# Optimization experiments

Hardware: AMD Instinct MI355X
Metric: run time of the kernel (lower is better)

## Reference

```python
import jax, jax.numpy as jnp
import numpy as np

N_NODES = 100000
N_EDGES = 1600000
D_IN = 13      # per-localization feature dim
D_POS = 3
HIDDEN = 64
D_OUT = 64


def setup_inputs() -> dict:
    key = jax.random.key(0)
    ks = jax.random.split(key, 6)
    x_locs = jax.random.normal(ks[0], (N_NODES, D_IN), dtype=jnp.float32)
    pos_locs = jax.random.uniform(ks[1], (N_NODES, D_POS), dtype=jnp.float32)
    edge_index = jax.random.randint(ks[2], (2, N_EDGES), 0, N_NODES, dtype=jnp.int64)
    fan1 = D_IN + D_POS
    W1 = jax.random.normal(ks[3], (fan1, HIDDEN), dtype=jnp.float32) / np.sqrt(fan1)
    b1 = jnp.zeros((HIDDEN,), dtype=jnp.float32)
    W2 = jax.random.normal(ks[4], (HIDDEN, D_OUT), dtype=jnp.float32) / np.sqrt(HIDDEN)
    b2 = jnp.zeros((D_OUT,), dtype=jnp.float32)
    return {"x_locs": x_locs, "pos_locs": pos_locs, "W1": W1, "b1": b1,
            "W2": W2, "b2": b2, "edge_index": edge_index}


def reference(x_locs, pos_locs, W1, b1, W2, b2, edge_index):
    # PointNetConv (source_to_target): j = edge_index[0] (source), i = edge_index[1] (target)
    src = edge_index[0]
    dst = edge_index[1]
    # message input: [x_j, pos_j - pos_i]  -> [E, D_IN + D_POS]
    msg_in = jnp.concatenate([x_locs[src], pos_locs[src] - pos_locs[dst]], axis=-1)
    # local_nn: Linear -> ReLU -> Linear
    h = jax.nn.relu(msg_in @ W1 + b1)            # [E, HIDDEN]
    h = h @ W2 + b2                               # [E, D_OUT]
    # max aggregation per target node; empty segments get -inf
    agg = jax.ops.segment_max(h, dst, num_segments=N_NODES)  # [N, D_OUT]
    # final .relu() in LocEncoder; also maps empty (-inf) segments to 0 (PyG convention)
    return jax.nn.relu(agg)
```

## Files before the change

### kernel.cpp

```cpp
#include <hip/hip_runtime.h>


#define N_NODES 100000
#define N_EDGES 1600000
#define NB2  1563
#define NBLK 391
#define BATCH 4096
#define SCAP2 1280

typedef _Float16 half8 __attribute__((ext_vector_type(8)));
typedef float float4v __attribute__((ext_vector_type(4)));

__device__ inline int wave_incl_scan(int v, int lane) {
#pragma unroll
    for (int d = 1; d < 64; d <<= 1) {
        const int t = __shfl_up(v, d);
        if (lane >= d) v += t;
    }
    return v;
}

__global__ __launch_bounds__(256) void precompute_kernel(
    const float* __restrict__ x, const float* __restrict__ pos,
    const float* __restrict__ W1, const float* __restrict__ b1,
    _Float16* __restrict__ u16, _Float16* __restrict__ w16)
{
    const int lane = threadIdx.x & 63;
    float w1c[16];
#pragma unroll
    for (int k = 0; k < 16; ++k) w1c[k] = W1[k * 64 + lane];
    const float b1c = b1[lane];

    const int waveId = blockIdx.x * 4 + (threadIdx.x >> 6);
    const int step   = 512 * 4 * 2;

    for (int nd = waveId * 2; nd < N_NODES; nd += step) {
        const int nA = nd, nB = nd + 1;
        float mA = 0.f, mB = 0.f;
        if (lane < 13) {
            mA = x[nA * 13 + lane];
            mB = x[nB * 13 + lane];
        } else if (lane < 16) {
            mA = pos[nA * 3 + (lane - 13)];
            mB = pos[nB * 3 + (lane - 13)];
        }

        float aA = b1c, wA = 0.f, aB = b1c, wB = 0.f;
#pragma unroll
        for (int k = 0; k < 13; ++k) {
            aA = fmaf(__shfl(mA, k), w1c[k], aA);
            aB = fmaf(__shfl(mB, k), w1c[k], aB);
        }
#pragma unroll
        for (int k = 13; k < 16; ++k) {
            const float pA = __shfl(mA, k), pB = __shfl(mB, k);
            aA = fmaf(pA, w1c[k], aA);  wA = fmaf(pA, w1c[k], wA);
            aB = fmaf(pB, w1c[k], aB);  wB = fmaf(pB, w1c[k], wB);
        }
        u16[nA * 64 + lane] = (_Float16)aA;
        w16[nA * 64 + lane] = (_Float16)wA;
        u16[nB * 64 + lane] = (_Float16)aB;
        w16[nB * 64 + lane] = (_Float16)wB;
    }
}

__global__ __launch_bounds__(256) void partition_kernel(
    const int* __restrict__ ei,
    int* __restrict__ offsT,
    int* __restrict__ blockSorted)
{
    __shared__ int hist[NB2], eoff[NB2], offc[NB2];
    __shared__ int csumP[25];

    const int tid  = threadIdx.x;
    const int lane = tid & 63;
    const int wv   = tid >> 6;
    const int blk  = blockIdx.x;
    const int e0   = blk * BATCH;
    const int nn   = (N_EDGES - e0) < BATCH ? (N_EDGES - e0) : BATCH;

    for (int i = tid; i < NB2; i += 256) hist[i] = 0;
    __syncthreads();

#pragma unroll
    for (int rep = 0; rep < 4; ++rep) {
        const int base = rep * 1024 + tid * 4;
        if (base < nn) {
            const int4 d4 = *(const int4*)(ei + N_EDGES + e0 + base);
            atomicAdd(&hist[d4.x >> 6], 1);
            atomicAdd(&hist[d4.y >> 6], 1);
            atomicAdd(&hist[d4.z >> 6], 1);
            atomicAdd(&hist[d4.w >> 6], 1);
        }
    }
    __syncthreads();

    for (int c = wv; c < 25; c += 4) {
        const int idx = c * 64 + lane;
        const int val = (idx < NB2) ? hist[idx] : 0;
        const int inc = wave_incl_scan(val, lane);
        if (idx < NB2) eoff[idx] = inc;
        if (lane == 63) csumP[c] = inc;
    }
    __syncthreads();
    if (tid == 0) {
        int a = 0;
#pragma unroll
        for (int c = 0; c < 25; ++c) { const int t = csumP[c]; csumP[c] = a; a += t; }
    }
    __syncthreads();
    for (int c = wv; c < 25; c += 4) {
        const int idx = c * 64 + lane;
        if (idx < NB2) eoff[idx] += csumP[c] - hist[idx];
    }
    __syncthreads();

    for (int b = tid; b < NB2; b += 256) {
        offsT[b * NBLK + blk] = eoff[b];
        offc[b] = eoff[b];
    }
    if (tid == 0) offsT[NB2 * NBLK + blk] = nn;
    __syncthreads();

    int* dstp = blockSorted + blk * BATCH;
#pragma unroll
    for (int rep = 0; rep < 4; ++rep) {
        const int base = rep * 1024 + tid * 4;
        if (base < nn) {
            const int4 s4 = *(const int4*)(ei + e0 + base);
            const int4 d4 = *(const int4*)(ei + N_EDGES + e0 + base);
            int p;
            p = atomicAdd(&offc[d4.x >> 6], 1); dstp[p] = (s4.x << 6) | (d4.x & 63);
            p = atomicAdd(&offc[d4.y >> 6], 1); dstp[p] = (s4.y << 6) | (d4.y & 63);
            p = atomicAdd(&offc[d4.z >> 6], 1); dstp[p] = (s4.z << 6) | (d4.z & 63);
            p = atomicAdd(&offc[d4.w >> 6], 1); dstp[p] = (s4.w << 6) | (d4.w & 63);
        }
    }
}

__global__ __launch_bounds__(256, 4) void aggregate_kernel(
    const _Float16* __restrict__ u16,
    const _Float16* __restrict__ w16,
    const float* __restrict__ W2,
    const float* __restrict__ b2,
    const int*   __restrict__ offsT,
    const int*   __restrict__ blockSorted,
    float*       __restrict__ out)
{
    __shared__ int staged[SCAP2];
    __shared__ int sortedL[SCAP2];
    __shared__ int E[NBLK], G[NBLK];
    __shared__ int hist[64], nstart[64], hoff[64];
    __shared__ int csum[8];
    __shared__ int totT;

    const int tid  = threadIdx.x;
    const int lane = tid & 63;
    const int wv   = tid >> 6;
    const int q = lane >> 4, n = lane & 15;
    const int b = blockIdx.x;
    const int node0 = b * 64;

    half8 w2f[2][4];
#pragma unroll
    for (int s = 0; s < 2; ++s)
#pragma unroll
        for (int t = 0; t < 4; ++t)
#pragma unroll
            for (int j = 0; j < 8; ++j)
                w2f[s][t][j] = (_Float16)W2[(s * 32 + q * 8 + j) * 64 + (n + 16 * t)];
    float b2c[4];
#pragma unroll
    for (int t = 0; t < 4; ++t) b2c[t] = b2[n + 16 * t];

    if (tid < 64) hist[tid] = 0;

    for (int r = tid; r < NBLK; r += 256) {
        const int lo = offsT[b * NBLK + r];
        const int hi = offsT[(b + 1) * NBLK + r];
        staged[r] = hi - lo;
        G[r] = r * BATCH + lo;
    }
    __syncthreads();
    for (int c = wv; c < 7; c += 4) {
        const int idx = c * 64 + lane;
        const int val = (idx < NBLK) ? staged[idx] : 0;
        const int inc = wave_incl_scan(val, lane);
        if (idx < NBLK) E[idx] = inc;
        if (lane == 63) csum[c] = inc;
    }
    __syncthreads();
    if (tid == 0) {
        int a = 0;
#pragma unroll
        for (int c = 0; c < 7; ++c) { const int t = csum[c]; csum[c] = a; a += t; }
        totT = a;
    }
    __syncthreads();
    for (int c = wv; c < 7; c += 4) {
        const int idx = c * 64 + lane;
        if (idx < NBLK) E[idx] += csum[c] - staged[idx];
    }
    __syncthreads();

    int T = totT; T = T < SCAP2 ? T : SCAP2;

    for (int i = tid; i < T; i += 256) {
        int lo = 0, hi = NBLK - 1;
#pragma unroll
        for (int s = 0; s < 9; ++s) {
            const int mid = (lo + hi + 1) >> 1;
            if (E[mid] <= i) lo = mid; else hi = mid - 1;
        }
        const int w = blockSorted[G[lo] + (i - E[lo])];
        staged[i] = w;
        atomicAdd(&hist[w & 63], 1);
    }
    __syncthreads();

    if (wv == 0) {
        const int v = hist[lane];
        const int inc = wave_incl_scan(v, lane);
        nstart[lane] = inc - v;
        hoff[lane]   = inc - v;
    }
    __syncthreads();
    for (int i = tid; i < T; i += 256) {
        const int w = staged[i];
        const int p = atomicAdd(&hoff[w & 63], 1);
        sortedL[p] = w >> 6;
    }
    __syncthreads();

    const half8 zero8 = {0, 0, 0, 0, 0, 0, 0, 0};

    auto compute = [&](int node, int2 sd, int src,
                       half8 ulo, half8 uhi, half8 wl, half8 wh) {
        float vmax[4] = {0.f, 0.f, 0.f, 0.f};
        int base = 0;
        while (true) {
            const int rows = (sd.y - base) < 16 ? (sd.y - base) : 16;
            if (rows > 0) {
                const half8 alo = __builtin_elementwise_max(ulo - wl, zero8);
                const half8 ahi = __builtin_elementwise_max(uhi - wh, zero8);
                float4v c2[4];
#pragma unroll
                for (int t = 0; t < 4; ++t) {
                    c2[t] = __builtin_amdgcn_mfma_f32_16x16x32_f16(
                        alo, w2f[0][t], (float4v){0.f, 0.f, 0.f, 0.f}, 0, 0, 0);
                    c2[t] = __builtin_amdgcn_mfma_f32_16x16x32_f16(
                        ahi, w2f[1][t], c2[t], 0, 0, 0);
                }
#pragma unroll
                for (int r = 0; r < 4; ++r) {
                    const int row = q * 4 + r;
#pragma unroll
                    for (int t = 0; t < 4; ++t) {
                        const float v = c2[t][r] + b2c[t];
                        if (row < rows) vmax[t] = fmaxf(vmax[t], v);
                    }
                }
            }
            base += 16;
            if (base >= sd.y) break;
            const int r2 = (sd.y - base) < 16 ? (sd.y - base) : 16;
            src = (n < r2) ? sortedL[sd.x + base + n] : 0;
            ulo = *(const half8*)(u16 + src * 64 + q * 8);
            uhi = *(const half8*)(u16 + src * 64 + 32 + q * 8);
        }
#pragma unroll
        for (int t = 0; t < 4; ++t) {
            vmax[t] = fmaxf(vmax[t], __shfl_xor(vmax[t], 16));
            vmax[t] = fmaxf(vmax[t], __shfl_xor(vmax[t], 32));
        }
        float v = vmax[0];
        v = (q == 1) ? vmax[1] : v;
        v = (q == 2) ? vmax[2] : v;
        v = (q == 3) ? vmax[3] : v;
        if (node < N_NODES) out[node * 64 + lane] = v;
    };

    const int nlbase = wv * 16;
#pragma unroll 1
    for (int g = 0; g < 16; g += 2) {
        const int nlA = nlbase + g, nlB = nlA + 1;
        const int nA = node0 + nlA, nB = node0 + nlB;
        const int2 sdA = {nstart[nlA], hist[nlA]};
        const int2 sdB = {nstart[nlB], hist[nlB]};
        const int nAc = nA < (N_NODES - 1) ? nA : (N_NODES - 1);
        const int nBc = nB < (N_NODES - 1) ? nB : (N_NODES - 1);

        const int rA = sdA.y < 16 ? sdA.y : 16;
        const int rB = sdB.y < 16 ? sdB.y : 16;
        const int srcA = (n < rA) ? sortedL[sdA.x + n] : 0;
        const int srcB = (n < rB) ? sortedL[sdB.x + n] : 0;

        const half8 ulA = *(const half8*)(u16 + srcA * 64 + q * 8);
        const half8 uhA = *(const half8*)(u16 + srcA * 64 + 32 + q * 8);
        const half8 wlA = *(const half8*)(w16 + nAc * 64 + q * 8);
        const half8 whA = *(const half8*)(w16 + nAc * 64 + 32 + q * 8);
        const half8 ulB = *(const half8*)(u16 + srcB * 64 + q * 8);
        const half8 uhB = *(const half8*)(u16 + srcB * 64 + 32 + q * 8);
        const half8 wlB = *(const half8*)(w16 + nBc * 64 + q * 8);
        const half8 whB = *(const half8*)(w16 + nBc * 64 + 32 + q * 8);

        compute(nA, sdA, srcA, ulA, uhA, wlA, whA);
        compute(nB, sdB, srcB, ulB, uhB, wlB, whB);
    }
}

extern "C" void kernel_launch(void* const* d_in, const int* in_sizes, int n_in,
                              void* d_out, int out_size, void* d_ws, size_t ws_size,
                              hipStream_t stream) {
    const float* x   = (const float*)d_in[0];
    const float* pos = (const float*)d_in[1];
    const float* W1  = (const float*)d_in[2];
    const float* b1  = (const float*)d_in[3];
    const float* W2  = (const float*)d_in[4];
    const float* b2  = (const float*)d_in[5];
    const int*   ei  = (const int*)d_in[6];

    char* ws = (char*)d_ws;
    int* blockSorted = (int*)(ws + 0);
    int* offsT       = (int*)(ws + 6406144);
    _Float16* u16 = (_Float16*)(ws + 8852480);
    _Float16* w16 = (_Float16*)(ws + 21652480);

    precompute_kernel<<<512, 256, 0, stream>>>(x, pos, W1, b1, u16, w16);
    partition_kernel<<<NBLK, 256, 0, stream>>>(ei, offsT, blockSorted);
    aggregate_kernel<<<NB2, 256, 0, stream>>>(
        u16, w16, W2, b2, offsT, blockSorted, (float*)d_out);
}
```

Baseline: 195.6 us.

## Stage partition output in LDS, use 256 partition blocks, split aggregate launch

The edge partition now runs on 256 blocks of 6272 edges, one block per CU. Each block scatters its bucketed edges into an LDS stage buffer and then writes them to global memory in coalesced order, instead of scattering directly to global. This lets the aggregate kernel compute per-bucket offsets with a single 256-wide scan and no multi-chunk loop. The precompute grid is doubled, and the aggregate kernel is launched twice over halves of the buckets, which adds launch overhead for no clear benefit.

```diff
diff --git a/kernel.cpp b/kernel.cpp
--- a/kernel.cpp
+++ b/kernel.cpp
@@ -3,9 +3,9 @@
 
 #define N_NODES 100000
 #define N_EDGES 1600000
-#define NB2  1563
-#define NBLK 391
-#define BATCH 4096
+#define NB2   1563
+#define PNBLK 256
+#define PBATCH 6272
 #define SCAP2 1280
 
 typedef _Float16 half8 __attribute__((ext_vector_type(8)));
@@ -32,7 +32,7 @@
     const float b1c = b1[lane];
 
     const int waveId = blockIdx.x * 4 + (threadIdx.x >> 6);
-    const int step   = 512 * 4 * 2;
+    const int step   = 1024 * 4 * 2;
 
     for (int nd = waveId * 2; nd < N_NODES; nd += step) {
         const int nA = nd, nB = nd + 1;
@@ -69,29 +69,29 @@
     int* __restrict__ offsT,
     int* __restrict__ blockSorted)
 {
-    __shared__ int hist[NB2], eoff[NB2], offc[NB2];
+    __shared__ int stage[PBATCH];
+    __shared__ int hist[NB2], offc[NB2];
     __shared__ int csumP[25];
 
     const int tid  = threadIdx.x;
     const int lane = tid & 63;
     const int wv   = tid >> 6;
     const int blk  = blockIdx.x;
-    const int e0   = blk * BATCH;
-    const int nn   = (N_EDGES - e0) < BATCH ? (N_EDGES - e0) : BATCH;
+    const int e0   = blk * PBATCH;
+    const int nn   = (N_EDGES - e0) < PBATCH ? (N_EDGES - e0) : PBATCH;
 
     for (int i = tid; i < NB2; i += 256) hist[i] = 0;
     __syncthreads();
 
-#pragma unroll
-    for (int rep = 0; rep < 4; ++rep) {
-        const int base = rep * 1024 + tid * 4;
-        if (base < nn) {
-            const int4 d4 = *(const int4*)(ei + N_EDGES + e0 + base);
-            atomicAdd(&hist[d4.x >> 6], 1);
-            atomicAdd(&hist[d4.y >> 6], 1);
-            atomicAdd(&hist[d4.z >> 6], 1);
-            atomicAdd(&hist[d4.w >> 6], 1);
-        }
+    const int4* d4p = (const int4*)(ei + N_EDGES + e0);
+    const int4* s4p = (const int4*)(ei + e0);
+    const int nq = nn >> 2;
+    for (int i = tid; i < nq; i += 256) {
+        const int4 d4 = d4p[i];
+        atomicAdd(&hist[d4.x >> 6], 1);
+        atomicAdd(&hist[d4.y >> 6], 1);
+        atomicAdd(&hist[d4.z >> 6], 1);
+        atomicAdd(&hist[d4.w >> 6], 1);
     }
     __syncthreads();
 
@@ -99,7 +99,7 @@
         const int idx = c * 64 + lane;
         const int val = (idx < NB2) ? hist[idx] : 0;
         const int inc = wave_incl_scan(val, lane);
-        if (idx < NB2) eoff[idx] = inc;
+        if (idx < NB2) offc[idx] = inc - val;
         if (lane == 63) csumP[c] = inc;
     }
     __syncthreads();
@@ -111,31 +111,27 @@
     __syncthreads();
     for (int c = wv; c < 25; c += 4) {
         const int idx = c * 64 + lane;
-        if (idx < NB2) eoff[idx] += csumP[c] - hist[idx];
-    }
-    __syncthreads();
-
-    for (int b = tid; b < NB2; b += 256) {
-        offsT[b * NBLK + blk] = eoff[b];
-        offc[b] = eoff[b];
-    }
-    if (tid == 0) offsT[NB2 * NBLK + blk] = nn;
-    __syncthreads();
-
-    int* dstp = blockSorted + blk * BATCH;
-#pragma unroll
-    for (int rep = 0; rep < 4; ++rep) {
-        const int base = rep * 1024 + tid * 4;
-        if (base < nn) {
-            const int4 s4 = *(const int4*)(ei + e0 + base);
-            const int4 d4 = *(const int4*)(ei + N_EDGES + e0 + base);
-            int p;
-            p = atomicAdd(&offc[d4.x >> 6], 1); dstp[p] = (s4.x << 6) | (d4.x & 63);
-            p = atomicAdd(&offc[d4.y >> 6], 1); dstp[p] = (s4.y << 6) | (d4.y & 63);
-            p = atomicAdd(&offc[d4.z >> 6], 1); dstp[p] = (s4.z << 6) | (d4.z & 63);
-            p = atomicAdd(&offc[d4.w >> 6], 1); dstp[p] = (s4.w << 6) | (d4.w & 63);
-        }
-    }
+        if (idx < NB2) offc[idx] += csumP[c];
+    }
+    __syncthreads();
+
+    for (int b = tid; b < NB2; b += 256) offsT[b * PNBLK + blk] = offc[b];
+    if (tid == 0) offsT[NB2 * PNBLK + blk] = nn;
+    __syncthreads();
+
+    for (int i = tid; i < nq; i += 256) {
+        const int4 s4 = s4p[i];
+        const int4 d4 = d4p[i];
+        int p;
+        p = atomicAdd(&offc[d4.x >> 6], 1); stage[p] = (s4.x << 6) | (d4.x & 63);
+        p = atomicAdd(&offc[d4.y >> 6], 1); stage[p] = (s4.y << 6) | (d4.y & 63);
+        p = atomicAdd(&offc[d4.z >> 6], 1); stage[p] = (s4.z << 6) | (d4.z & 63);
+        p = atomicAdd(&offc[d4.w >> 6], 1); stage[p] = (s4.w << 6) | (d4.w & 63);
+    }
+    __syncthreads();
+
+    for (int i = tid; i < nn; i += 256)
+        blockSorted[e0 + i] = stage[i];
 }
 
 __global__ __launch_bounds__(256, 4) void aggregate_kernel(
@@ -145,20 +141,21 @@
     const float* __restrict__ b2,
     const int*   __restrict__ offsT,
     const int*   __restrict__ blockSorted,
-    float*       __restrict__ out)
+    float*       __restrict__ out,
+    int bucketBase)
 {
     __shared__ int staged[SCAP2];
     __shared__ int sortedL[SCAP2];
-    __shared__ int E[NBLK], G[NBLK];
+    __shared__ int E[PNBLK], G[PNBLK];
     __shared__ int hist[64], nstart[64], hoff[64];
-    __shared__ int csum[8];
+    __shared__ int csum[4];
     __shared__ int totT;
 
     const int tid  = threadIdx.x;
     const int lane = tid & 63;
     const int wv   = tid >> 6;
     const int q = lane >> 4, n = lane & 15;
-    const int b = blockIdx.x;
+    const int b = blockIdx.x + bucketBase;
     const int node0 = b * 64;
 
     half8 w2f[2][4];
@@ -175,40 +172,32 @@
 
     if (tid < 64) hist[tid] = 0;
 
-    for (int r = tid; r < NBLK; r += 256) {
-        const int lo = offsT[b * NBLK + r];
-        const int hi = offsT[(b + 1) * NBLK + r];
-        staged[r] = hi - lo;
-        G[r] = r * BATCH + lo;
-    }
-    __syncthreads();
-    for (int c = wv; c < 7; c += 4) {
-        const int idx = c * 64 + lane;
-        const int val = (idx < NBLK) ? staged[idx] : 0;
-        const int inc = wave_incl_scan(val, lane);
-        if (idx < NBLK) E[idx] = inc;
-        if (lane == 63) csum[c] = inc;
-    }
-    __syncthreads();
-    if (tid == 0) {
-        int a = 0;
-#pragma unroll
-        for (int c = 0; c < 7; ++c) { const int t = csum[c]; csum[c] = a; a += t; }
-        totT = a;
-    }
-    __syncthreads();
-    for (int c = wv; c < 7; c += 4) {
-        const int idx = c * 64 + lane;
-        if (idx < NBLK) E[idx] += csum[c] - staged[idx];
+    {
+        const int lo = offsT[b * PNBLK + tid];
+        const int hi = offsT[(b + 1) * PNBLK + tid];
+        const int len = hi - lo;
+        G[tid] = tid * PBATCH + lo;
+        const int inc = wave_incl_scan(len, lane);
+        E[tid] = inc;
+        if (lane == 63) csum[wv] = inc;
+        __syncthreads();
+        if (tid == 0) {
+            int a = 0;
+#pragma unroll
+            for (int c = 0; c < 4; ++c) { const int t = csum[c]; csum[c] = a; a += t; }
+            totT = a;
+        }
+        __syncthreads();
+        E[tid] += csum[wv] - len;
     }
     __syncthreads();
 
     int T = totT; T = T < SCAP2 ? T : SCAP2;
 
     for (int i = tid; i < T; i += 256) {
-        int lo = 0, hi = NBLK - 1;
-#pragma unroll
-        for (int s = 0; s < 9; ++s) {
+        int lo = 0, hi = PNBLK - 1;
+#pragma unroll
+        for (int s = 0; s < 8; ++s) {
             const int mid = (lo + hi + 1) >> 1;
             if (E[mid] <= i) lo = mid; else hi = mid - 1;
         }
@@ -322,12 +311,14 @@
 
     char* ws = (char*)d_ws;
     int* blockSorted = (int*)(ws + 0);
-    int* offsT       = (int*)(ws + 6406144);
-    _Float16* u16 = (_Float16*)(ws + 8852480);
-    _Float16* w16 = (_Float16*)(ws + 21652480);
-
-    precompute_kernel<<<512, 256, 0, stream>>>(x, pos, W1, b1, u16, w16);
-    partition_kernel<<<NBLK, 256, 0, stream>>>(ei, offsT, blockSorted);
-    aggregate_kernel<<<NB2, 256, 0, stream>>>(
-        u16, w16, W2, b2, offsT, blockSorted, (float*)d_out);
-}
+    int* offsT       = (int*)(ws + 6400000);
+    _Float16* u16 = (_Float16*)(ws + 8001536);
+    _Float16* w16 = (_Float16*)(ws + 20801536);
+
+    precompute_kernel<<<1024, 256, 0, stream>>>(x, pos, W1, b1, u16, w16);
+    partition_kernel<<<PNBLK, 256, 0, stream>>>(ei, offsT, blockSorted);
+    aggregate_kernel<<<782, 256, 0, stream>>>(
+        u16, w16, W2, b2, offsT, blockSorted, (float*)d_out, 0);
+    aggregate_kernel<<<781, 256, 0, stream>>>(
+        u16, w16, W2, b2, offsT, blockSorted, (float*)d_out, 782);
+}
```

Result: no change. 196.1 us (+0.3%).
